# Kernel tuning notes

Measured on AMD Instinct MI355X. Metric: run time of the kernel, lower is better.

Reference implementation:

```python
import jax, jax.numpy as jnp
import numpy as np

B, N, C = 32, 577, 1024
NUM_HEADS = 16
HEAD_DIM = C // NUM_HEADS
SCALE = HEAD_DIM ** -0.5
HW = 24          # sqrt(N-1)
POOL = 8         # AdaptiveAvgPool2d output size
KS = HW // POOL  # exact 3x3 average pooling


def setup_inputs() -> dict:
    key = jax.random.key(0)
    k1, k2, k3 = jax.random.split(key, 3)
    X = jax.random.normal(k1, (B, N, C), dtype=jnp.float32)
    W_qkv = jax.random.normal(k2, (3 * C, C), dtype=jnp.float32) * (C ** -0.5)
    W_proj = jax.random.normal(k3, (C, C), dtype=jnp.float32) * (C ** -0.5)
    b_proj = jnp.zeros((C,), dtype=jnp.float32)
    return {"X": X, "W_qkv": W_qkv, "W_proj": W_proj, "b_proj": b_proj, "layer_idx": 1}


def reference(X, W_qkv, W_proj, b_proj, layer_idx):
    # layer_idx <= 100 branch: two-stage pooled-query attention
    qkv = X @ W_qkv.T                              # [B, N, 3C]
    Xq, Xk, Xv = jnp.split(qkv, 3, axis=-1)        # each [B, N, C]

    # Adaptive avg-pool the non-cls query tokens to an 8x8 grid (exact 3x3 mean)
    Qp = Xq[:, :-1, :].reshape(B, POOL, KS, POOL, KS, C).mean(axis=(2, 4))  # [B,8,8,C]
    Qp = Qp.reshape(B, POOL * POOL, C)             # [B, 64, C]

    def to_heads(t, L):
        return t.reshape(B, L, NUM_HEADS, HEAD_DIM).transpose(0, 2, 1, 3)

    Qh = to_heads(Xq, N)       # [B, H, N, d]
    Kh = to_heads(Xk, N)
    Vh = to_heads(Xv, N)
    Q = to_heads(Qp, POOL * POOL)  # [B, H, 64, d]

    # Stage 1: pooled queries cross-attend to full K/V
    s1 = jnp.einsum('bhqd,bhkd->bhqk', Q * SCALE, Kh)   # [B,H,64,N]
    A1 = jax.nn.softmax(s1, axis=-1)
    Q_delta = jnp.einsum('bhqk,bhkd->bhqd', A1, Vh)     # [B,H,64,d]

    # Stage 2: original queries attend to pooled queries, read Q_delta
    s2 = jnp.einsum('bhnd,bhqd->bhnq', Qh * SCALE, Q)   # [B,H,N,64]
    A2 = jax.nn.softmax(s2, axis=-1)
    out = jnp.einsum('bhnq,bhqd->bhnd', A2, Q_delta)    # [B,H,N,d]

    out = out.transpose(0, 2, 1, 3).reshape(B, N, C)
    return out @ W_proj.T + b_proj
```

## Files before the change

kernel.cpp:

```cpp
#include <hip/hip_runtime.h>

typedef unsigned short u16;
typedef u16 u16x8 __attribute__((ext_vector_type(8)));
typedef u16 u16x4 __attribute__((ext_vector_type(4)));
typedef __bf16 bf16x8 __attribute__((ext_vector_type(8)));
typedef float f32x4 __attribute__((ext_vector_type(4)));

#define DEVI static __device__ __forceinline__

#define BB 32
#define NN 577
#define CC 1024
#define HH 16
#define DD 64
#define MM (BB * NN)
#define SCALE_ 0.125f

DEVI u16 f2bf(float f) {
  union { float f; unsigned u; } v; v.f = f;
  unsigned r = v.u + 0x7FFFu + ((v.u >> 16) & 1u);
  return (u16)(r >> 16);
}
DEVI float bf2f(u16 b) {
  union { unsigned u; float f; } v; v.u = ((unsigned)b) << 16; return v.f;
}
DEVI f32x4 mfma16(u16x8 a, u16x8 b, f32x4 c) {
  return __builtin_amdgcn_mfma_f32_16x16x32_bf16(
      __builtin_bit_cast(bf16x8, a), __builtin_bit_cast(bf16x8, b), c, 0, 0, 0);
}
DEVI void gload_lds16(const u16* g, u16* l) {
  __builtin_amdgcn_global_load_lds(
      (const __attribute__((address_space(1))) void*)g,
      (__attribute__((address_space(3))) void*)l, 16, 0, 0);
}

__global__ void cvt3_kernel(const float* __restrict__ X, const float* __restrict__ Wq,
                            const float* __restrict__ Wp, u16* __restrict__ Xb,
                            u16* __restrict__ Wqb, u16* __restrict__ Wpb) {
  const int nX = (MM * CC) / 4;
  const int nQ = (3 * CC * CC) / 4;
  const int nP = (CC * CC) / 4;
  const int total = nX + nQ + nP;
  int i = blockIdx.x * blockDim.x + threadIdx.x;
  int stride = gridDim.x * blockDim.x;
  for (; i < total; i += stride) {
    const float* in; u16* out; int k;
    if (i < nX)            { in = X;  out = Xb;  k = i; }
    else if (i < nX + nQ)  { in = Wq; out = Wqb; k = i - nX; }
    else                   { in = Wp; out = Wpb; k = i - nX - nQ; }
    float4 v = ((const float4*)in)[k];
    u16x4 o = { f2bf(v.x), f2bf(v.y), f2bf(v.z), f2bf(v.w) };
    ((u16x4*)out)[k] = o;
  }
}

__global__ __launch_bounds__(256) void gemm_bt2(
    const u16* __restrict__ A, const u16* __restrict__ Bw,
    u16* __restrict__ Cb, float* __restrict__ Cf, const float* __restrict__ bias,
    int M, int N, int K, int MT, int NT)
{
  __shared__ u16 Als[128 * 64];
  __shared__ u16 Bls[128 * 64];

  int nwg = MT * NT;
  int orig = blockIdx.x;
  int q = nwg >> 3, r = nwg & 7;
  int xcd = orig & 7, idx = orig >> 3;
  int wg = (xcd < r ? xcd * (q + 1) : r * (q + 1) + (xcd - r) * q) + idx;
  int mt = wg / NT, nt = wg % NT;

  const int t = threadIdx.x, lane = t & 63, w = t >> 6;
  const int wr = (w >> 1) * 64, wc = (w & 1) * 64;
  const int fr = lane & 15, fg = lane >> 4;
  const int m0 = mt * 128, n0 = nt * 128;
  f32x4 acc[4][4] = {};

  const int swcol = ((lane & 7) ^ ((lane >> 3) & 7)) * 8;
  const u16* pA[4];
  const u16* pB[4];
#pragma unroll
  for (int i = 0; i < 4; ++i) {
    int row = w * 32 + i * 8 + (lane >> 3);
    int ga = m0 + row; if (ga > M - 1) ga = M - 1;
    pA[i] = A + (size_t)ga * K + swcol;
    pB[i] = Bw + (size_t)(n0 + row) * K + swcol;
  }

  for (int kt = 0; kt < K; kt += 64) {
#pragma unroll
    for (int i = 0; i < 4; ++i) {
      int c = w * 4 + i;
      gload_lds16(pA[i] + kt, &Als[c * 512]);
      gload_lds16(pB[i] + kt, &Bls[c * 512]);
    }
    __syncthreads();
#pragma unroll
    for (int kk = 0; kk < 2; ++kk) {
      u16x8 af[4], bfr[4];
#pragma unroll
      for (int m = 0; m < 4; ++m) {
        int row = wr + m * 16 + fr;
        int ch = (kk * 4 + fg) ^ (fr & 7);
        af[m] = *(const u16x8*)&Als[row * 64 + ch * 8];
      }
#pragma unroll
      for (int n = 0; n < 4; ++n) {
        int row = wc + n * 16 + fr;
        int ch = (kk * 4 + fg) ^ (fr & 7);
        bfr[n] = *(const u16x8*)&Bls[row * 64 + ch * 8];
      }
#pragma unroll
      for (int m = 0; m < 4; ++m)
#pragma unroll
        for (int n = 0; n < 4; ++n)
          acc[m][n] = mfma16(af[m], bfr[n], acc[m][n]);
    }
    __syncthreads();
  }

#pragma unroll
  for (int m = 0; m < 4; ++m) {
#pragma unroll
    for (int j = 0; j < 4; ++j) {
      int row = m0 + wr + m * 16 + fg * 4 + j;
      if (row >= M) continue;
#pragma unroll
      for (int n = 0; n < 4; ++n) {
        int col = n0 + wc + n * 16 + fr;
        float v = acc[m][n][j];
        if (Cf) Cf[(size_t)row * N + col] = v + bias[col];
        else    Cb[(size_t)row * N + col] = f2bf(v);
      }
    }
  }
}

__global__ __launch_bounds__(256) void attn_fused(
    const u16* __restrict__ qkv, u16* __restrict__ AO)
{
  __shared__ u16 Qp[64][72];
  __shared__ u16 Qd[64][72];
  __shared__ u16 Kls[64][72];
  __shared__ u16 Vt[64][72];
  __shared__ u16 Pls[4][16][72];

  int bh = blockIdx.x, b = bh >> 4, h = bh & 15;
  int t = threadIdx.x, lane = t & 63, w = t >> 6;
  int fr = lane & 15, fg = lane >> 4;

  {
    int pq = t >> 2, d0 = (t & 3) * 16;
    int py = pq >> 3, px = pq & 7;
    float s[16] = {};
#pragma unroll
    for (int dy = 0; dy < 3; ++dy)
#pragma unroll
      for (int dx = 0; dx < 3; ++dx) {
        int n = (py * 3 + dy) * 24 + px * 3 + dx;
        const u16* p = qkv + (size_t)(b * NN + n) * 3072 + h * DD + d0;
        u16x8 v0 = *(const u16x8*)p;
        u16x8 v1 = *(const u16x8*)(p + 8);
#pragma unroll
        for (int j = 0; j < 8; ++j) { s[j] += bf2f(v0[j]); s[8 + j] += bf2f(v1[j]); }
      }
    const float rinv = 1.f / 9.f;
    u16x8 o0, o1;
#pragma unroll
    for (int j = 0; j < 8; ++j) { o0[j] = f2bf(s[j] * rinv); o1[j] = f2bf(s[8 + j] * rinv); }
    *(u16x8*)&Qp[pq][d0] = o0;
    *(u16x8*)&Qp[pq][d0 + 8] = o1;
  }
  __syncthreads();

  {
    u16x8 qf0 = *(const u16x8*)&Qp[w * 16 + fr][fg * 8];
    u16x8 qf1 = *(const u16x8*)&Qp[w * 16 + fr][32 + fg * 8];

    f32x4 o[4] = {};
    float rowm[4] = {-1e30f, -1e30f, -1e30f, -1e30f};
    float rowl[4] = {};

    for (int kt = 0; kt < 10; ++kt) {
#pragma unroll
      for (int i = 0; i < 2; ++i) {
        int g = t + i * 256;
        int key = g >> 3, cc = (g & 7) * 8;
        int n = kt * 64 + key;
        u16x8 kv = {}, vv = {};
        if (n < NN) {
          const u16* p = qkv + (size_t)(b * NN + n) * 3072 + h * DD + cc;
          kv = *(const u16x8*)(p + CC);
          vv = *(const u16x8*)(p + 2 * CC);
        }
        *(u16x8*)&Kls[key][cc] = kv;
#pragma unroll
        for (int j = 0; j < 8; ++j) Vt[cc + j][key] = vv[j];
      }
      __syncthreads();

      f32x4 s[4] = {};
#pragma unroll
      for (int kk = 0; kk < 2; ++kk) {
        u16x8 qf = kk ? qf1 : qf0;
#pragma unroll
        for (int n = 0; n < 4; ++n) {
          u16x8 kf = *(const u16x8*)&Kls[n * 16 + fr][kk * 32 + fg * 8];
          s[n] = mfma16(qf, kf, s[n]);
        }
      }
      float mx[4] = {-1e30f, -1e30f, -1e30f, -1e30f};
#pragma unroll
      for (int n = 0; n < 4; ++n) {
        int key = kt * 64 + n * 16 + fr;
#pragma unroll
        for (int j = 0; j < 4; ++j) {
          float v = s[n][j] * SCALE_;
          if (key >= NN) v = -1e30f;
          s[n][j] = v;
          mx[j] = fmaxf(mx[j], v);
        }
      }
      for (int d = 1; d < 16; d <<= 1) {
#pragma unroll
        for (int j = 0; j < 4; ++j) mx[j] = fmaxf(mx[j], __shfl_xor(mx[j], d));
      }
      float corr[4];
#pragma unroll
      for (int j = 0; j < 4; ++j) {
        float mn = fmaxf(rowm[j], mx[j]);
        corr[j] = __expf(rowm[j] - mn);
        rowm[j] = mn;
      }
      float rs[4] = {};
#pragma unroll
      for (int n = 0; n < 4; ++n)
#pragma unroll
        for (int j = 0; j < 4; ++j) {
          float p = __expf(s[n][j] - rowm[j]);
          s[n][j] = p;
          rs[j] += p;
        }
      for (int d = 1; d < 16; d <<= 1) {
#pragma unroll
        for (int j = 0; j < 4; ++j) rs[j] += __shfl_xor(rs[j], d);
      }
#pragma unroll
      for (int j = 0; j < 4; ++j) rowl[j] = rowl[j] * corr[j] + rs[j];
#pragma unroll
      for (int n = 0; n < 4; ++n)
#pragma unroll
        for (int j = 0; j < 4; ++j) o[n][j] *= corr[j];

#pragma unroll
      for (int n = 0; n < 4; ++n)
#pragma unroll
        for (int j = 0; j < 4; ++j)
          Pls[w][fg * 4 + j][n * 16 + fr] = f2bf(s[n][j]);

#pragma unroll
      for (int kk = 0; kk < 2; ++kk) {
        u16x8 pf = *(const u16x8*)&Pls[w][fr][kk * 32 + fg * 8];
#pragma unroll
        for (int n = 0; n < 4; ++n) {
          u16x8 vf = *(const u16x8*)&Vt[n * 16 + fr][kk * 32 + fg * 8];
          o[n] = mfma16(pf, vf, o[n]);
        }
      }
      __syncthreads();
    }

#pragma unroll
    for (int n = 0; n < 4; ++n)
#pragma unroll
      for (int j = 0; j < 4; ++j)
        Qd[n * 16 + fr][w * 16 + fg * 4 + j] = f2bf(o[n][j] / rowl[j]);
  }
  __syncthreads();

  u16x8 bq[2][4], dq[2][4];
#pragma unroll
  for (int kk = 0; kk < 2; ++kk)
#pragma unroll
    for (int n = 0; n < 4; ++n) {
      bq[kk][n] = *(const u16x8*)&Qp[n * 16 + fr][kk * 32 + fg * 8];
      dq[kk][n] = *(const u16x8*)&Qd[n * 16 + fr][kk * 32 + fg * 8];
    }

  for (int nt = 0; nt < 10; ++nt) {
    int n0 = nt * 64;
    int qrow = n0 + w * 16 + fr;
    int qc = qrow < NN ? qrow : NN - 1;
    const u16* Qb = qkv + (size_t)(b * NN + qc) * 3072 + h * DD;
    u16x8 a0 = *(const u16x8*)(Qb + fg * 8);
    u16x8 a1 = *(const u16x8*)(Qb + 32 + fg * 8);

    f32x4 s[4] = {};
#pragma unroll
    for (int n = 0; n < 4; ++n) {
      s[n] = mfma16(a0, bq[0][n], s[n]);
      s[n] = mfma16(a1, bq[1][n], s[n]);
    }
    float mx[4] = {-1e30f, -1e30f, -1e30f, -1e30f};
#pragma unroll
    for (int n = 0; n < 4; ++n)
#pragma unroll
      for (int j = 0; j < 4; ++j) {
        float v = s[n][j] * SCALE_;
        s[n][j] = v;
        mx[j] = fmaxf(mx[j], v);
      }
    for (int d = 1; d < 16; d <<= 1) {
#pragma unroll
      for (int j = 0; j < 4; ++j) mx[j] = fmaxf(mx[j], __shfl_xor(mx[j], d));
    }
    float rs[4] = {};
#pragma unroll
    for (int n = 0; n < 4; ++n)
#pragma unroll
      for (int j = 0; j < 4; ++j) {
        float p = __expf(s[n][j] - mx[j]);
        s[n][j] = p;
        rs[j] += p;
      }
    for (int d = 1; d < 16; d <<= 1) {
#pragma unroll
      for (int j = 0; j < 4; ++j) rs[j] += __shfl_xor(rs[j], d);
    }

#pragma unroll
    for (int n = 0; n < 4; ++n)
#pragma unroll
      for (int j = 0; j < 4; ++j)
        Pls[w][fg * 4 + j][n * 16 + fr] = f2bf(s[n][j]);

    f32x4 of[4] = {};
#pragma unroll
    for (int kk = 0; kk < 2; ++kk) {
      u16x8 pf = *(const u16x8*)&Pls[w][fr][kk * 32 + fg * 8];
#pragma unroll
      for (int n = 0; n < 4; ++n)
        of[n] = mfma16(pf, dq[kk][n], of[n]);
    }

#pragma unroll
    for (int n = 0; n < 4; ++n)
#pragma unroll
      for (int j = 0; j < 4; ++j) {
        int orow = n0 + w * 16 + fg * 4 + j;
        if (orow < NN)
          AO[(size_t)(b * NN + orow) * CC + h * DD + n * 16 + fr] = f2bf(of[n][j] / rs[j]);
      }
  }
}

extern "C" void kernel_launch(void* const* d_in, const int* in_sizes, int n_in,
                              void* d_out, int out_size, void* d_ws, size_t ws_size,
                              hipStream_t stream) {
  const float* X     = (const float*)d_in[0];
  const float* Wqkv  = (const float*)d_in[1];
  const float* Wproj = (const float*)d_in[2];
  const float* bproj = (const float*)d_in[3];

  char* ws = (char*)d_ws;
  u16* Xb  = (u16*)(ws + 0);
  u16* Wqb = (u16*)(ws + 37814272);
  u16* Wpb = (u16*)(ws + 44105728);
  u16* qkv = (u16*)(ws + 46202880);
  u16* AO  = (u16*)(ws + 159645696);

  cvt3_kernel<<<2048, 256, 0, stream>>>(X, Wqkv, Wproj, Xb, Wqb, Wpb);

  gemm_bt2<<<145 * 24, 256, 0, stream>>>(Xb, Wqb, qkv, nullptr, nullptr,
                                         MM, 3 * CC, CC, 145, 24);

  attn_fused<<<BB * HH, 256, 0, stream>>>(qkv, AO);

  gemm_bt2<<<145 * 8, 256, 0, stream>>>(AO, Wpb, nullptr, (float*)d_out, bproj,
                                        MM, CC, CC, 145, 8);
}
```

Baseline: 295.3 us.

## Use 256x256-tile 8-wave ping-pong GEMM for the QKV projection

Adds a new bf16 GEMM kernel with 256x256 output tiles, 512 threads (8 waves), and double-buffered LDS. Each k-step is split into four phases that interleave direct global-to-LDS loads of the next tiles with MFMA work, using barriers and s_setprio to stagger the waves. The QKV projection GEMM now uses this kernel, which raises per-workgroup data reuse and overlaps memory traffic with compute. In exchange it runs one workgroup per CU with high register pressure, and 73 M-tiles leave padding waste on the last tile.

```diff
diff --git a/kernel.cpp b/kernel.cpp
--- a/kernel.cpp
+++ b/kernel.cpp
@@ -33,6 +33,8 @@
       (const __attribute__((address_space(1))) void*)g,
       (__attribute__((address_space(3))) void*)l, 16, 0, 0);
 }
+DEVI void fencec() { asm volatile("" ::: "memory"); }
+DEVI void lbar() { fencec(); __builtin_amdgcn_s_barrier(); fencec(); }
 
 __global__ void cvt3_kernel(const float* __restrict__ X, const float* __restrict__ Wq,
                             const float* __restrict__ Wp, u16* __restrict__ Xb,
@@ -54,6 +56,162 @@
   }
 }
 
+__global__ __launch_bounds__(512, 1) void gemm_8p(
+    const u16* __restrict__ A, const u16* __restrict__ Bw,
+    u16* __restrict__ Cb, int M, int N, int K, int MT, int NT)
+{
+  __shared__ u16 Als[2][16384];
+  __shared__ u16 Bls[2][16384];
+
+  int nwg = MT * NT;
+  int orig = blockIdx.x;
+  int q = nwg >> 3, r = nwg & 7;
+  int xcd = orig & 7, idx = orig >> 3;
+  int wg = (xcd < r ? xcd * (q + 1) : r * (q + 1) + (xcd - r) * q) + idx;
+  int mt = wg / NT, nt = wg % NT;
+
+  const int t = threadIdx.x, lane = t & 63, w = t >> 6;
+  const int wr2 = w >> 2, wc2 = w & 3;
+  const int fr = lane & 15, fg = lane >> 4;
+  const int m0 = mt * 256, n0 = nt * 256;
+
+  f32x4 acc[8][4] = {};
+
+  const int swcol = ((lane & 7) ^ ((lane >> 3) & 7)) * 8;
+  const u16* pA[2][2];
+  const u16* pB[2][2];
+#pragma unroll
+  for (int h = 0; h < 2; ++h)
+#pragma unroll
+    for (int j = 0; j < 2; ++j) {
+      int row = h * 128 + (w * 2 + j) * 8 + (lane >> 3);
+      int ga = m0 + row; if (ga > M - 1) ga = M - 1;
+      pA[h][j] = A + (size_t)ga * K + swcol;
+      pB[h][j] = Bw + (size_t)(n0 + row) * K + swcol;
+    }
+  const int lofs = (w * 2) * 512;
+
+  auto stageA = [&](int tile, int h, int buf) {
+    const int kc = tile << 6;
+    gload_lds16(pA[h][0] + kc, &Als[buf][h * 8192 + lofs]);
+    gload_lds16(pA[h][1] + kc, &Als[buf][h * 8192 + lofs + 512]);
+  };
+  auto stageB = [&](int tile, int h, int buf) {
+    const int kc = tile << 6;
+    gload_lds16(pB[h][0] + kc, &Bls[buf][h * 8192 + lofs]);
+    gload_lds16(pB[h][1] + kc, &Bls[buf][h * 8192 + lofs + 512]);
+  };
+
+  const int chk[2] = { ((0 * 4 + fg) ^ (fr & 7)) * 8, ((1 * 4 + fg) ^ (fr & 7)) * 8 };
+  const int arow = wr2 * 128 + fr;
+  const int brow = wc2 * 64 + fr;
+
+  const int nkt = K >> 6;
+
+  stageA(0, 0, 0); stageA(0, 1, 0);
+  stageB(0, 0, 0); stageB(0, 1, 0);
+  stageA(1, 0, 1); stageA(1, 1, 1);
+  asm volatile("s_waitcnt vmcnt(4)" ::: "memory");
+  lbar();
+
+  u16x8 aL[4][2], aH[4][2], bL[2][2], bH[2][2];
+
+  for (int T = 0; T < nkt; ++T) {
+    const int cur = T & 1, nxt = cur ^ 1;
+    const u16* Ac = &Als[cur][0];
+    const u16* Bc = &Bls[cur][0];
+    const bool s1 = (T + 1 < nkt), s2 = (T + 2 < nkt);
+
+#pragma unroll
+    for (int m = 0; m < 4; ++m)
+#pragma unroll
+      for (int kk = 0; kk < 2; ++kk)
+        aL[m][kk] = *(const u16x8*)&Ac[(arow + m * 16) * 64 + chk[kk]];
+#pragma unroll
+    for (int n = 0; n < 2; ++n)
+#pragma unroll
+      for (int kk = 0; kk < 2; ++kk)
+        bL[n][kk] = *(const u16x8*)&Bc[(brow + n * 16) * 64 + chk[kk]];
+    if (s1) stageB(T + 1, 0, nxt);
+    lbar();
+    __builtin_amdgcn_s_setprio(1);
+#pragma unroll
+    for (int m = 0; m < 4; ++m)
+#pragma unroll
+      for (int n = 0; n < 2; ++n)
+#pragma unroll
+        for (int kk = 0; kk < 2; ++kk)
+          acc[m][n] = mfma16(aL[m][kk], bL[n][kk], acc[m][n]);
+    __builtin_amdgcn_s_setprio(0);
+    lbar();
+
+#pragma unroll
+    for (int m = 0; m < 4; ++m)
+#pragma unroll
+      for (int kk = 0; kk < 2; ++kk)
+        aH[m][kk] = *(const u16x8*)&Ac[(arow + (m + 4) * 16) * 64 + chk[kk]];
+    if (s1) stageB(T + 1, 1, nxt);
+    lbar();
+    __builtin_amdgcn_s_setprio(1);
+#pragma unroll
+    for (int m = 0; m < 4; ++m)
+#pragma unroll
+      for (int n = 0; n < 2; ++n)
+#pragma unroll
+        for (int kk = 0; kk < 2; ++kk)
+          acc[m + 4][n] = mfma16(aH[m][kk], bL[n][kk], acc[m + 4][n]);
+    __builtin_amdgcn_s_setprio(0);
+    lbar();
+
+#pragma unroll
+    for (int n = 0; n < 2; ++n)
+#pragma unroll
+      for (int kk = 0; kk < 2; ++kk)
+        bH[n][kk] = *(const u16x8*)&Bc[(brow + (n + 2) * 16) * 64 + chk[kk]];
+    if (s2) stageA(T + 2, 0, cur);
+    lbar();
+    __builtin_amdgcn_s_setprio(1);
+#pragma unroll
+    for (int m = 0; m < 4; ++m)
+#pragma unroll
+      for (int n = 0; n < 2; ++n)
+#pragma unroll
+        for (int kk = 0; kk < 2; ++kk)
+          acc[m][n + 2] = mfma16(aL[m][kk], bH[n][kk], acc[m][n + 2]);
+    __builtin_amdgcn_s_setprio(0);
+    lbar();
+
+    if (s2) stageA(T + 2, 1, cur);
+    lbar();
+    __builtin_amdgcn_s_setprio(1);
+#pragma unroll
+    for (int m = 0; m < 4; ++m)
+#pragma unroll
+      for (int n = 0; n < 2; ++n)
+#pragma unroll
+        for (int kk = 0; kk < 2; ++kk)
+          acc[m + 4][n + 2] = mfma16(aH[m][kk], bH[n][kk], acc[m + 4][n + 2]);
+    __builtin_amdgcn_s_setprio(0);
+    if (s2) asm volatile("s_waitcnt vmcnt(4)" ::: "memory");
+    else    asm volatile("s_waitcnt vmcnt(0)" ::: "memory");
+    lbar();
+  }
+
+#pragma unroll
+  for (int m = 0; m < 8; ++m) {
+#pragma unroll
+    for (int j = 0; j < 4; ++j) {
+      int row = m0 + wr2 * 128 + m * 16 + fg * 4 + j;
+      if (row >= M) continue;
+#pragma unroll
+      for (int n = 0; n < 4; ++n) {
+        int col = n0 + wc2 * 64 + n * 16 + fr;
+        Cb[(size_t)row * N + col] = f2bf(acc[m][n][j]);
+      }
+    }
+  }
+}
+
 __global__ __launch_bounds__(256) void gemm_bt2(
     const u16* __restrict__ A, const u16* __restrict__ Bw,
     u16* __restrict__ Cb, float* __restrict__ Cf, const float* __restrict__ bias,
@@ -370,8 +528,7 @@
 
   cvt3_kernel<<<2048, 256, 0, stream>>>(X, Wqkv, Wproj, Xb, Wqb, Wpb);
 
-  gemm_bt2<<<145 * 24, 256, 0, stream>>>(Xb, Wqb, qkv, nullptr, nullptr,
-                                         MM, 3 * CC, CC, 145, 24);
+  gemm_8p<<<73 * 12, 512, 0, stream>>>(Xb, Wqb, qkv, MM, 3 * CC, CC, 73, 12);
 
   attn_fused<<<BB * HH, 256, 0, stream>>>(qkv, AO);
 
```

Measured after the change: 285.1 us. -3.4%, faster.
